# Optimization experiments

Hardware: AMD Instinct MI355X
Metric: run time of the kernel (lower is better)

The kernel has to match this reference:

```python
import jax, jax.numpy as jnp
import numpy as np

IM_SIZE = 128  # imSize: image is [B,1,IM_SIZE,IM_SIZE]


def setup_inputs() -> dict:
    key = jax.random.key(0)
    # channel 0: image to reconstruct; channel 1: passthrough 'others' channel
    inp = jax.random.normal(key, (16, 2, IM_SIZE, IM_SIZE), dtype=jnp.float32)
    return {"input": inp}


def reference(input):
    S = IM_SIZE
    x = input[:, 0]        # [B,H,W] real image (input[:, :1] in torch)
    others = input[:, 1:]  # extra channels, concatenated back at the end

    # RFFT: torch.rfft(x, 2, onesided=False, normalized=False) == fft2
    K = jnp.fft.fft2(x)    # [B,H,W] complex64

    # seperate_mask keeps only k-space column i for output channel i:
    # masked[b,i,h,w] = K[b,h,w] * (w == i)
    eye = jnp.eye(S, dtype=jnp.float32)
    masked = K[:, None, :, :] * eye[None, :, None, :]  # [B,S,H,W]

    # IFFT: torch.ifft(..., normalized=False) == standard 1/N-normalized ifft2;
    # module keeps channel 0 of the (real, imag) pair -> real part.
    imgs = jnp.fft.ifft2(masked).real.astype(input.dtype)  # [B,S,H,W]

    return jnp.concatenate([imgs, others], axis=1)  # [B, S + C-1, H, W]
```

## Files before the change

kernel.cpp:

```cpp
#include <hip/hip_runtime.h>
#include <math.h>

#define S 128
#define NB 16
constexpr float STEP = 6.283185307179586f / 128.0f;

typedef float f32x4 __attribute__((ext_vector_type(4)));

__global__ void dft_rows(const float* __restrict__ in, float2* __restrict__ Ft) {
    const int by = blockIdx.x;
    const int b  = by >> 7;
    const int y  = by & (S - 1);
    const int s  = threadIdx.x;

    __shared__ float  row[S];
    __shared__ float2 tw[S];
    row[s] = in[((b * 2 + 0) * S + y) * S + s];
    float sn, cs;
    __sincosf((float)s * STEP, &sn, &cs);
    tw[s] = make_float2(cs, sn);
    __syncthreads();

    float re = 0.f, im = 0.f;
#pragma unroll 8
    for (int v = 0; v < S; ++v) {
        const int k = (s * v) & (S - 1);
        const float2 t = tw[k];
        const float xv = row[v];
        re = fmaf(xv,  t.x, re);
        im = fmaf(xv, -t.y, im);
    }
    Ft[(b * S + s) * S + y] = make_float2(re, im);
}

__global__ void modulate(const float2* __restrict__ Ft, const float* __restrict__ in,
                         float* __restrict__ out) {
    const int blk = blockIdx.x;
    const int t   = threadIdx.x;

    if (blk >= NB * S) {
        const int b = blk - NB * S;
        const f32x4* src = (const f32x4*)&in[((b * 2 + 1) * S) * S];
        f32x4*       dst = (f32x4*)&out[((b * 129 + S) * S) * S];
#pragma unroll
        for (int i = 0; i < 16; ++i) {
            const f32x4 v = src[i * 256 + t];
            __builtin_nontemporal_store(v, &dst[i * 256 + t]);
        }
        return;
    }

    const int b = blk >> 7;
    const int s = blk & (S - 1);

    __shared__ float2 Fs[S];
    __shared__ float  cosT[S], sinT[S];
    if (t < S) {
        Fs[t] = Ft[(b * S + s) * S + t];
        float sn, cs;
        __sincosf((float)t * STEP, &sn, &cs);
        cosT[t] = cs;
        sinT[t] = sn;
    }
    __syncthreads();

    const int x0 = (t & 31) * 4;
    const int y0 = t >> 5;

    float mc[4], ms[4];
#pragma unroll
    for (int j = 0; j < 4; ++j) {
        const int k = (s * (x0 + j)) & (S - 1);
        mc[j] = cosT[k];
        ms[j] = sinT[k];
    }

    float2 fv[16];
#pragma unroll
    for (int i = 0; i < 16; ++i)
        fv[i] = Fs[y0 + i * 8];

    float* obase = &out[((b * 129 + s) * S) * S];
#pragma unroll
    for (int i = 0; i < 16; ++i) {
        const int y = y0 + i * 8;
        const float re = fv[i].x * (1.0f / S);
        const float im = fv[i].y * (1.0f / S);
        f32x4 o;
        o.x = re * mc[0] - im * ms[0];
        o.y = re * mc[1] - im * ms[1];
        o.z = re * mc[2] - im * ms[2];
        o.w = re * mc[3] - im * ms[3];
        __builtin_nontemporal_store(o, (f32x4*)&obase[y * S + x0]);
    }
}

extern "C" void kernel_launch(void* const* d_in, const int* in_sizes, int n_in,
                              void* d_out, int out_size, void* d_ws, size_t ws_size,
                              hipStream_t stream) {
    const float* in  = (const float*)d_in[0];
    float*       out = (float*)d_out;
    float2*      Ft  = (float2*)d_ws;

    dft_rows<<<NB * S, S, 0, stream>>>(in, Ft);
    modulate<<<NB * S + NB, 256, 0, stream>>>(Ft, in, out);
}
```

Baseline: 154.5 us.

## Fuse row DFT and modulation into one kernel with recurrence twiddles

Merges the two kernels into a single launch. Each 1024-thread block stages one full image in padded shared memory, computes the row DFT for 4 frequency columns using a rotating-twiddle recurrence split into two halves, then writes the modulated outputs. This removes the intermediate global buffer, the second launch, and the table lookups. The cost is that each image is reloaded from global memory 32 times, shared memory use rises to about 66KB per block, and the recurrence accumulates some float rounding error.

```diff
diff --git a/kernel.cpp b/kernel.cpp
--- a/kernel.cpp
+++ b/kernel.cpp
@@ -3,95 +3,96 @@
 
 #define S 128
 #define NB 16
+#define PITCH 129
 constexpr float STEP = 6.283185307179586f / 128.0f;
 
 typedef float f32x4 __attribute__((ext_vector_type(4)));
 
-__global__ void dft_rows(const float* __restrict__ in, float2* __restrict__ Ft) {
-    const int by = blockIdx.x;
-    const int b  = by >> 7;
-    const int y  = by & (S - 1);
-    const int s  = threadIdx.x;
-
-    __shared__ float  row[S];
-    __shared__ float2 tw[S];
-    row[s] = in[((b * 2 + 0) * S + y) * S + s];
-    float sn, cs;
-    __sincosf((float)s * STEP, &sn, &cs);
-    tw[s] = make_float2(cs, sn);
-    __syncthreads();
-
-    float re = 0.f, im = 0.f;
-#pragma unroll 8
-    for (int v = 0; v < S; ++v) {
-        const int k = (s * v) & (S - 1);
-        const float2 t = tw[k];
-        const float xv = row[v];
-        re = fmaf(xv,  t.x, re);
-        im = fmaf(xv, -t.y, im);
-    }
-    Ft[(b * S + s) * S + y] = make_float2(re, im);
-}
-
-__global__ void modulate(const float2* __restrict__ Ft, const float* __restrict__ in,
-                         float* __restrict__ out) {
+__global__ __launch_bounds__(1024, 8)
+void kspace_fused(const float* __restrict__ in, float* __restrict__ out) {
     const int blk = blockIdx.x;
     const int t   = threadIdx.x;
 
-    if (blk >= NB * S) {
-        const int b = blk - NB * S;
-        const f32x4* src = (const f32x4*)&in[((b * 2 + 1) * S) * S];
-        f32x4*       dst = (f32x4*)&out[((b * 129 + S) * S) * S];
+    if (blk >= NB * 32) {
+        const int b = blk - NB * 32;
+        const f32x4* src = (const f32x4*)&in[(b * 2 + 1) * S * S];
+        f32x4*       dst = (f32x4*)&out[(b * 129 + S) * S * S];
 #pragma unroll
-        for (int i = 0; i < 16; ++i) {
-            const f32x4 v = src[i * 256 + t];
-            __builtin_nontemporal_store(v, &dst[i * 256 + t]);
+        for (int i = 0; i < 4; ++i) {
+            const f32x4 v = src[t + i * 1024];
+            __builtin_nontemporal_store(v, &dst[t + i * 1024]);
         }
         return;
     }
 
-    const int b = blk >> 7;
-    const int s = blk & (S - 1);
+    const int b  = blk >> 5;
+    const int sq = blk & 31;
 
-    __shared__ float2 Fs[S];
-    __shared__ float  cosT[S], sinT[S];
-    if (t < S) {
-        Fs[t] = Ft[(b * S + s) * S + t];
-        float sn, cs;
-        __sincosf((float)t * STEP, &sn, &cs);
-        cosT[t] = cs;
-        sinT[t] = sn;
+    __shared__ float  img[S * PITCH];
+    __shared__ float2 part[4][2][S];
+
+    {
+        const f32x4* src = (const f32x4*)&in[(b * 2) * S * S];
+#pragma unroll
+        for (int i = 0; i < 4; ++i) {
+            const int fidx = t + i * 1024;
+            const f32x4 v = src[fidx];
+            const int y = fidx >> 5;
+            const int c = fidx & 31;
+            float* p = &img[y * PITCH + c * 4];
+            p[0] = v.x; p[1] = v.y; p[2] = v.z; p[3] = v.w;
+        }
     }
     __syncthreads();
 
+    const int s_local = t >> 8;
+    const int s       = sq * 4 + s_local;
+    const int y       = t & 127;
+    const int half    = (t >> 7) & 1;
+
+    float sn1, cs1;
+    __sincosf((float)s * STEP, &sn1, &cs1);
+
+    float wRe = half ? ((s & 1) ? -1.f : 1.f) : 1.f;
+    float wIm = 0.f;
+    float accRe = 0.f, accIm = 0.f;
+    const float* row = &img[y * PITCH + half * 64];
+#pragma unroll 8
+    for (int v = 0; v < 64; ++v) {
+        const float xv = row[v];
+        accRe = fmaf(xv, wRe, accRe);
+        accIm = fmaf(xv, wIm, accIm);
+        const float nRe = fmaf(wRe, cs1,  wIm * sn1);
+        const float nIm = fmaf(wIm, cs1, -wRe * sn1);
+        wRe = nRe; wIm = nIm;
+    }
+    part[s_local][half][y] = make_float2(accRe, accIm);
+    __syncthreads();
+
     const int x0 = (t & 31) * 4;
-    const int y0 = t >> 5;
+    const int y0 = (t >> 5) & 7;
 
     float mc[4], ms[4];
 #pragma unroll
     for (int j = 0; j < 4; ++j) {
         const int k = (s * (x0 + j)) & (S - 1);
-        mc[j] = cosT[k];
-        ms[j] = sinT[k];
+        __sincosf((float)k * STEP, &ms[j], &mc[j]);
     }
-
-    float2 fv[16];
-#pragma unroll
-    for (int i = 0; i < 16; ++i)
-        fv[i] = Fs[y0 + i * 8];
 
     float* obase = &out[((b * 129 + s) * S) * S];
 #pragma unroll
     for (int i = 0; i < 16; ++i) {
-        const int y = y0 + i * 8;
-        const float re = fv[i].x * (1.0f / S);
-        const float im = fv[i].y * (1.0f / S);
+        const int yy = y0 + i * 8;
+        const float2 p0 = part[s_local][0][yy];
+        const float2 p1 = part[s_local][1][yy];
+        const float fRe = (p0.x + p1.x) * (1.0f / S);
+        const float fIm = (p0.y + p1.y) * (1.0f / S);
         f32x4 o;
-        o.x = re * mc[0] - im * ms[0];
-        o.y = re * mc[1] - im * ms[1];
-        o.z = re * mc[2] - im * ms[2];
-        o.w = re * mc[3] - im * ms[3];
-        __builtin_nontemporal_store(o, (f32x4*)&obase[y * S + x0]);
+        o.x = fRe * mc[0] - fIm * ms[0];
+        o.y = fRe * mc[1] - fIm * ms[1];
+        o.z = fRe * mc[2] - fIm * ms[2];
+        o.w = fRe * mc[3] - fIm * ms[3];
+        __builtin_nontemporal_store(o, (f32x4*)&obase[yy * S + x0]);
     }
 }
 
@@ -100,8 +101,5 @@
                               hipStream_t stream) {
     const float* in  = (const float*)d_in[0];
     float*       out = (float*)d_out;
-    float2*      Ft  = (float2*)d_ws;
-
-    dft_rows<<<NB * S, S, 0, stream>>>(in, Ft);
-    modulate<<<NB * S + NB, 256, 0, stream>>>(Ft, in, out);
+    kspace_fused<<<NB * 32 + NB, 1024, 0, stream>>>(in, out);
 }
```

Result: faster. 150.6 us (-2.5%).

## Split modulate blocks in half, drop shared memory, use regular stores

Applied to the files above, without the earlier changes.

Doubles the modulate grid so each block writes half of a 128x128 output image, and splits the passthrough copy across two blocks as well. Each thread now loads its 8 consecutive Ft values directly from global memory as vector loads and computes its own sincos twiddles, which removes the shared-memory staging and the __syncthreads. Nontemporal stores are replaced with ordinary stores. The aim is more parallelism and less per-block latency on a kernel bound by output writes, at the cost of redundant sincos work and different cache behaviour on the stores.

```diff
diff --git a/kernel.cpp b/kernel.cpp
--- a/kernel.cpp
+++ b/kernel.cpp
@@ -33,65 +33,53 @@
     Ft[(b * S + s) * S + y] = make_float2(re, im);
 }
 
-__global__ void modulate(const float2* __restrict__ Ft, const float* __restrict__ in,
-                         float* __restrict__ out) {
+__global__ __launch_bounds__(256)
+void modulate(const float2* __restrict__ Ft, const float* __restrict__ in,
+              float* __restrict__ out) {
     const int blk = blockIdx.x;
     const int t   = threadIdx.x;
 
-    if (blk >= NB * S) {
-        const int b = blk - NB * S;
-        const f32x4* src = (const f32x4*)&in[((b * 2 + 1) * S) * S];
-        f32x4*       dst = (f32x4*)&out[((b * 129 + S) * S) * S];
+    if (blk >= NB * S * 2) {
+        const int idx = blk - NB * S * 2;
+        const int b = idx >> 1, h = idx & 1;
+        const f32x4* src = (const f32x4*)&in[(b * 2 + 1) * S * S] + h * 2048;
+        f32x4*       dst = (f32x4*)&out[(b * 129 + S) * S * S] + h * 2048;
 #pragma unroll
-        for (int i = 0; i < 16; ++i) {
-            const f32x4 v = src[i * 256 + t];
-            __builtin_nontemporal_store(v, &dst[i * 256 + t]);
-        }
+        for (int i = 0; i < 8; ++i)
+            dst[t + i * 256] = src[t + i * 256];
         return;
     }
 
-    const int b = blk >> 7;
-    const int s = blk & (S - 1);
-
-    __shared__ float2 Fs[S];
-    __shared__ float  cosT[S], sinT[S];
-    if (t < S) {
-        Fs[t] = Ft[(b * S + s) * S + t];
-        float sn, cs;
-        __sincosf((float)t * STEP, &sn, &cs);
-        cosT[t] = cs;
-        sinT[t] = sn;
-    }
-    __syncthreads();
+    const int b = blk >> 8;
+    const int s = (blk >> 1) & (S - 1);
+    const int h = blk & 1;
 
     const int x0 = (t & 31) * 4;
-    const int y0 = t >> 5;
+    const int yb = h * 64 + (t >> 5) * 8;
+
+    union { f32x4 q[4]; float2 v[8]; } F;
+    const f32x4* Fp = (const f32x4*)&Ft[(b * S + s) * S + yb];
+#pragma unroll
+    for (int i = 0; i < 4; ++i) F.q[i] = Fp[i];
 
     float mc[4], ms[4];
 #pragma unroll
     for (int j = 0; j < 4; ++j) {
         const int k = (s * (x0 + j)) & (S - 1);
-        mc[j] = cosT[k];
-        ms[j] = sinT[k];
+        __sincosf((float)k * STEP, &ms[j], &mc[j]);
     }
-
-    float2 fv[16];
-#pragma unroll
-    for (int i = 0; i < 16; ++i)
-        fv[i] = Fs[y0 + i * 8];
 
     float* obase = &out[((b * 129 + s) * S) * S];
 #pragma unroll
-    for (int i = 0; i < 16; ++i) {
-        const int y = y0 + i * 8;
-        const float re = fv[i].x * (1.0f / S);
-        const float im = fv[i].y * (1.0f / S);
+    for (int i = 0; i < 8; ++i) {
+        const float re = F.v[i].x * (1.0f / S);
+        const float im = F.v[i].y * (1.0f / S);
         f32x4 o;
         o.x = re * mc[0] - im * ms[0];
         o.y = re * mc[1] - im * ms[1];
         o.z = re * mc[2] - im * ms[2];
         o.w = re * mc[3] - im * ms[3];
-        __builtin_nontemporal_store(o, (f32x4*)&obase[y * S + x0]);
+        *(f32x4*)&obase[(yb + i) * S + x0] = o;
     }
 }
 
@@ -103,5 +91,5 @@
     float2*      Ft  = (float2*)d_ws;
 
     dft_rows<<<NB * S, S, 0, stream>>>(in, Ft);
-    modulate<<<NB * S + NB, 256, 0, stream>>>(Ft, in, out);
+    modulate<<<NB * S * 2 + NB * 2, 256, 0, stream>>>(Ft, in, out);
 }
```

Result: faster. 145.4 us (-5.9%).
